# Performance work log

Hardware: AMD Instinct MI355X
Metric: run time of the kernel (lower is better)

Reference implementation:

```python
import jax, jax.numpy as jnp
import numpy as np

D_STATE = 128   # Mamba2 default (the SS2D d_state=16 is never forwarded to Mamba2)
N_HEADS = 4     # d_ssm // headdim = d_model / (d_model//4)
D_CONV = 4
EPS = 1e-5


def silu(v):
    return v * jax.nn.sigmoid(v)


def setup_inputs() -> dict:
    key = jax.random.key(0)
    ks = jax.random.split(key, 12)
    d_model = 256
    d_inner = 2 * d_model            # expand=2
    d_ssm = d_model
    conv_dim = d_ssm + 2 * D_STATE   # 512
    d_in_proj = 2 * d_inner + 2 * D_STATE + N_HEADS  # 1284
    B, H, W = 8, 64, 64
    inp = {
        "x": jax.random.normal(ks[0], (B, d_model, H, W), jnp.float32),
        "in_proj_w": jax.random.normal(ks[1], (d_in_proj, d_model), jnp.float32) * 0.02,
        "conv_w": jax.random.normal(ks[2], (conv_dim, D_CONV), jnp.float32) * 0.2,
        "conv_b": jnp.zeros((conv_dim,), jnp.float32),
        "dt_bias": jax.random.normal(ks[3], (N_HEADS,), jnp.float32) * 0.1,
        "A_log": jnp.log(jax.random.uniform(ks[4], (N_HEADS,), jnp.float32, 1.0, 16.0)),
        "D": jax.random.normal(ks[5], (N_HEADS,), jnp.float32),
        "norm_w": jnp.ones((d_ssm,), jnp.float32),
        "out_proj_w": jax.random.normal(ks[6], (d_model, d_inner), jnp.float32) * 0.02,
        "se_w1": jax.random.normal(ks[7], (d_model // 4, d_model), jnp.float32) * 0.05,
        "se_b1": jnp.zeros((d_model // 4,), jnp.float32),
        "se_w2": jax.random.normal(ks[8], (d_model, d_model // 4), jnp.float32) * 0.05,
        "se_b2": jnp.zeros((d_model,), jnp.float32),
    }
    return inp


def _forward(x, in_proj_w, conv_w, conv_b, dt_bias, A_log, D, norm_w,
             out_proj_w, se_w1, se_b1, se_w2, se_b2):
    Bb, C, H, W = x.shape
    L = H * W
    d_model = C
    d_inner = 2 * d_model
    d_ssm = d_model
    d_mlp = d_inner - d_ssm
    headdim = d_ssm // N_HEADS
    conv_dim = d_ssm + 2 * D_STATE

    u = x.reshape(Bb, C, L).transpose(0, 2, 1)              # (b, l, c)
    zxbcdt = u @ in_proj_w.T                                 # (b, l, 1284)
    z0 = zxbcdt[..., :d_mlp]
    x0 = zxbcdt[..., d_mlp:2 * d_mlp]
    z = zxbcdt[..., 2 * d_mlp:2 * d_mlp + d_ssm]
    xBC = zxbcdt[..., 2 * d_mlp + d_ssm:2 * d_mlp + d_ssm + conv_dim]
    dt = zxbcdt[..., -N_HEADS:]

    dt = jax.nn.softplus(dt + dt_bias)                       # (b, l, h)

    # causal depthwise conv along l, kernel size D_CONV
    xpad = jnp.pad(xBC, ((0, 0), (D_CONV - 1, 0), (0, 0)))
    xconv = conv_b
    for k in range(D_CONV):
        xconv = xconv + xpad[:, k:k + L, :] * conv_w[:, k]
    xconv = silu(xconv)

    xs = xconv[..., :d_ssm]
    Bm = xconv[..., d_ssm:d_ssm + D_STATE]                   # (b, l, n) ngroups=1
    Cm = xconv[..., d_ssm + D_STATE:]                        # (b, l, n)
    xh = xs.reshape(Bb, L, N_HEADS, headdim)                 # (b, l, h, p)

    A = -jnp.exp(A_log)                                      # (h,)

    def step(hstate, inp):
        xt, dtt, Bt, Ct = inp  # (b,h,p), (b,h), (b,n), (b,n)
        dA = jnp.exp(dtt * A)                                # (b, h)
        hstate = hstate * dA[:, :, None, None] + \
            (dtt[:, :, None, None] * xt[..., None]) * Bt[:, None, None, :]
        y = jnp.einsum('bhpn,bn->bhp', hstate, Ct)
        return hstate, y

    h0 = jnp.zeros((Bb, N_HEADS, headdim, D_STATE), x.dtype)
    _, ys = jax.lax.scan(
        step, h0,
        (xh.transpose(1, 0, 2, 3), dt.transpose(1, 0, 2),
         Bm.transpose(1, 0, 2), Cm.transpose(1, 0, 2)))
    y = ys.transpose(1, 0, 2, 3)                             # (b, l, h, p)
    y = y + D[None, None, :, None] * xh                      # skip
    y = y.reshape(Bb, L, d_ssm)

    # gated RMSNorm (norm_before_gate=False): gate then normalize
    y = y * silu(z)
    y = y * jax.lax.rsqrt(jnp.mean(y * y, axis=-1, keepdims=True) + EPS) * norm_w

    y = jnp.concatenate([silu(z0) * x0, y], axis=-1)         # (b, l, d_inner)
    out = y @ out_proj_w.T                                   # (b, l, d_model)
    out = out.transpose(0, 2, 1).reshape(Bb, C, H, W)

    # SE-style spectral attention
    s = out.mean(axis=(2, 3))                                # (b, c)
    s = jax.nn.relu(s @ se_w1.T + se_b1)
    s = jax.nn.sigmoid(s @ se_w2.T + se_b2)
    return out * s[:, :, None, None]


def reference(x, in_proj_w, conv_w, conv_b, dt_bias, A_log, D, norm_w,
              out_proj_w, se_w1, se_b1, se_w2, se_b2):
    return _forward(x, in_proj_w, conv_w, conv_b, dt_bias, A_log, D, norm_w,
                    out_proj_w, se_w1, se_b1, se_w2, se_b2)
```

## Files before the change

kernel.cpp:

```cpp
#include <hip/hip_runtime.h>
#include <stdint.h>

typedef __attribute__((ext_vector_type(8))) short bf16x8;
typedef __attribute__((ext_vector_type(4))) float f32x4;

__device__ __forceinline__ float bf2f(unsigned short u) {
  unsigned int x = ((unsigned int)u) << 16;
  return __builtin_bit_cast(float, x);
}
__device__ __forceinline__ unsigned short f2bf(float f) {
  unsigned int x = __builtin_bit_cast(unsigned int, f);
  unsigned int r = x + 0x7FFFu + ((x >> 16) & 1u);
  return (unsigned short)(r >> 16);
}
__device__ __forceinline__ float silu(float v) { return v / (1.f + expf(-v)); }
__device__ __forceinline__ f32x4 fz4() { f32x4 z; z[0]=0.f; z[1]=0.f; z[2]=0.f; z[3]=0.f; return z; }

#define LSEQ 4096
#define DMODEL 256
#define NIN 1284
#define NINP 1408

__global__ void k_prep_w(const float* __restrict__ w_in, const float* __restrict__ w_out,
                         unsigned short* __restrict__ wpad, unsigned short* __restrict__ woutbf) {
  int idx = blockIdx.x * 256 + threadIdx.x;
  const int tot1 = NINP * DMODEL;
  if (idx < tot1) {
    int n = idx / DMODEL, k = idx % DMODEL;
    float v = (n < NIN) ? w_in[n * DMODEL + k] : 0.f;
    wpad[idx] = f2bf(v);
  } else {
    int j = idx - tot1;
    woutbf[j] = f2bf(w_out[j]);
  }
}

__global__ __launch_bounds__(256) void k_transpose_x(const float* __restrict__ x,
                                                     unsigned short* __restrict__ ubf) {
  __shared__ float t[64][65];
  int bid = blockIdx.x;
  int b = bid >> 8;
  int r = bid & 255;
  int lt = r >> 2, kt = r & 3;
  int l0 = lt * 64, k0 = kt * 64;
  int tid = threadIdx.x;
  int j = tid & 63, i0 = tid >> 6;
  for (int rr = 0; rr < 16; rr++) {
    int ki = i0 + rr * 4;
    t[ki][j] = x[(size_t)(b * DMODEL + k0 + ki) * LSEQ + l0 + j];
  }
  __syncthreads();
  for (int rr = 0; rr < 16; rr++) {
    int li = i0 + rr * 4;
    ubf[(size_t)(b * LSEQ + l0 + li) * DMODEL + k0 + j] = f2bf(t[j][li]);
  }
}

template <int KDIM, int LDA, int LDB, int EPI>
__global__ __launch_bounds__(256) void k_gemm(const unsigned short* __restrict__ A,
                                              const unsigned short* __restrict__ B,
                                              float* __restrict__ outF,
                                              unsigned short* __restrict__ outBF,
                                              unsigned short* __restrict__ outBF2,
                                              float* __restrict__ dtb, int tilesN) {
  __shared__ __align__(16) short lds[17408];
  short* As = lds;
  short* Bs = lds + 8192;
  int nwg = gridDim.x;
  int orig = blockIdx.x;
  int wgid = (nwg & 7) ? orig : ((orig & 7) * (nwg >> 3) + (orig >> 3));
  int tn = wgid % tilesN, tm = wgid / tilesN;
  int m0 = tm * 128, n0 = tn * 128;
  int tid = threadIdx.x;
  int w = tid >> 6, lane = tid & 63;
  int wr = w >> 1, wc = w & 1;
  f32x4 acc[4][4];
  for (int i = 0; i < 4; i++)
    for (int j = 0; j < 4; j++) acc[i][j] = fz4();

  for (int kt = 0; kt < KDIM / 64; kt++) {
    int k0 = kt * 64;
    for (int i = 0; i < 4; i++) {
      int rowblk = w * 32 + i * 8;
      int row = rowblk + (lane >> 3);
      int kc = (lane & 7) * 8;
      const unsigned short* ga = A + (size_t)(m0 + row) * LDA + k0 + kc;
      __builtin_amdgcn_global_load_lds((const __attribute__((address_space(1))) unsigned int*)ga,
                                       (__attribute__((address_space(3))) unsigned int*)&As[rowblk * 64],
                                       16, 0, 0);
      const unsigned short* gb = B + (size_t)(n0 + row) * LDB + k0 + kc;
      __builtin_amdgcn_global_load_lds((const __attribute__((address_space(1))) unsigned int*)gb,
                                       (__attribute__((address_space(3))) unsigned int*)&Bs[rowblk * 64],
                                       16, 0, 0);
    }
    __syncthreads();
    for (int kk = 0; kk < 64; kk += 32) {
      bf16x8 af[4], bfr[4];
      for (int mi = 0; mi < 4; mi++)
        af[mi] = *(const bf16x8*)&As[(wr * 64 + mi * 16 + (lane & 15)) * 64 + kk + (lane >> 4) * 8];
      for (int ni = 0; ni < 4; ni++)
        bfr[ni] = *(const bf16x8*)&Bs[(wc * 64 + ni * 16 + (lane & 15)) * 64 + kk + (lane >> 4) * 8];
      for (int mi = 0; mi < 4; mi++)
        for (int ni = 0; ni < 4; ni++)
          acc[mi][ni] = __builtin_amdgcn_mfma_f32_16x16x32_bf16(af[mi], bfr[ni], acc[mi][ni], 0, 0, 0);
    }
    __syncthreads();
  }

  int fq = lane >> 4, fr = lane & 15;
  if constexpr (EPI == 1) {
    float* Cf = (float*)lds;
    for (int ph = 0; ph < 2; ph++) {
      if (ph) __syncthreads();
      if (wc == ph) {
        for (int mi = 0; mi < 4; mi++)
          for (int ni = 0; ni < 4; ni++)
            for (int j = 0; j < 4; j++)
              Cf[(wr * 64 + mi * 16 + fq * 4 + j) * 68 + ni * 16 + fr] = acc[mi][ni][j];
      }
      __syncthreads();
      int rr = tid >> 4, cc = (tid & 15) * 4;
      for (int it = 0; it < 8; it++) {
        int r = it * 16 + rr;
        float4 v = *(const float4*)&Cf[r * 68 + cc];
        *(float4*)&outF[(size_t)(m0 + r) * 256 + n0 + ph * 64 + cc] = v;
      }
    }
  } else {
    bool dttile = (n0 >= 1280);
    if (dttile) {
      if (wc == 0 && fr < 4) {
        for (int mi = 0; mi < 4; mi++)
          for (int j = 0; j < 4; j++) {
            int m = m0 + wr * 64 + mi * 16 + fq * 4 + j;
            dtb[m * 4 + fr] = acc[mi][0][j];
          }
      }
    } else {
      short* Ct = lds;
      for (int mi = 0; mi < 4; mi++)
        for (int ni = 0; ni < 4; ni++)
          for (int j = 0; j < 4; j++)
            Ct[(wr * 64 + mi * 16 + fq * 4 + j) * 136 + wc * 64 + ni * 16 + fr] =
                (short)f2bf(acc[mi][ni][j]);
      __syncthreads();
      int rr = tid >> 4, cc = (tid & 15) * 8;
      for (int it = 0; it < 8; it++) {
        int r = it * 16 + rr;
        uint4 v = *(const uint4*)&Ct[r * 136 + cc];
        if constexpr (EPI == 0) {
          *(uint4*)&outBF[(size_t)(m0 + r) * 1280 + n0 + cc] = v;
        } else {
          if (n0 < 768) *(uint4*)&outBF[(size_t)(m0 + r) * 768 + n0 + cc] = v;
          else *(uint4*)&outBF2[(size_t)(m0 + r) * 512 + (n0 - 768) + cc] = v;
        }
      }
    }
  }
}

__global__ __launch_bounds__(256) void k_conv(const unsigned short* __restrict__ src, int stride,
                                              const float* __restrict__ conv_w,
                                              const float* __restrict__ conv_b,
                                              unsigned short* __restrict__ xs,
                                              unsigned short* __restrict__ bc) {
  __shared__ __align__(16) unsigned short xt[35 * 512];
  int bid = blockIdx.x;
  int b = bid >> 7;
  int t0 = (bid & 127) * 32;
  int tid = threadIdx.x;
  for (int id = tid; id < 35 * 64; id += 256) {
    int r = id >> 6, ch = id & 63;
    int t = t0 - 3 + r;
    float4 v;
    if (t < 0) v = make_float4(0.f, 0.f, 0.f, 0.f);
    else v = *(const float4*)&src[(size_t)(b * LSEQ + t) * stride + ch * 8];
    *(float4*)&xt[r * 512 + ch * 8] = v;
  }
  __syncthreads();
  int c0 = tid, c1 = tid + 256;
  float w0[4], w1[4];
  for (int k = 0; k < 4; k++) { w0[k] = conv_w[c0 * 4 + k]; w1[k] = conv_w[c1 * 4 + k]; }
  float bb0 = conv_b[c0], bb1 = conv_b[c1];
  for (int tl = 0; tl < 32; tl++) {
    float a0 = bb0, a1 = bb1;
    for (int k = 0; k < 4; k++) {
      a0 += bf2f(xt[(tl + k) * 512 + c0]) * w0[k];
      a1 += bf2f(xt[(tl + k) * 512 + c1]) * w1[k];
    }
    a0 = silu(a0); a1 = silu(a1);
    size_t row = (size_t)(b * LSEQ + t0 + tl);
    xs[row * 256 + c0] = f2bf(a0);
    bc[row * 256 + (c1 - 256)] = f2bf(a1);
  }
}

__global__ __launch_bounds__(256) void k_scan(const unsigned short* __restrict__ xs,
                                              const unsigned short* __restrict__ bc,
                                              const float* __restrict__ dtb,
                                              const float* __restrict__ dt_bias,
                                              const float* __restrict__ A_log,
                                              const float* __restrict__ Dp,
                                              unsigned short* __restrict__ y) {
  __shared__ __align__(16) unsigned short bcl[32 * 256];
  __shared__ float xsl[32][4];
  __shared__ float dtl[32], dal[32];
  int bid = blockIdx.x;
  int b = bid >> 6;
  int h = (bid >> 4) & 3;
  int pg = bid & 15;
  int tid = threadIdx.x, w = tid >> 6, lane = tid & 63;
  int p = pg * 4 + w;
  float Ah = -expf(A_log[h]);
  float Dh = Dp[h];
  float bias = dt_bias[h];
  float h0 = 0.f, h1 = 0.f;
  for (int t0 = 0; t0 < LSEQ; t0 += 32) {
    for (int id = tid; id < 32 * 32; id += 256) {
      int r = id >> 5, ch = id & 31;
      *(float4*)&bcl[r * 256 + ch * 8] =
          *(const float4*)&bc[(size_t)(b * LSEQ + t0 + r) * 256 + ch * 8];
    }
    if (tid < 128) {
      int r = tid >> 2, pp = tid & 3;
      xsl[r][pp] = bf2f(xs[(size_t)(b * LSEQ + t0 + r) * 256 + h * 64 + pg * 4 + pp]);
    } else if (tid < 160) {
      int r = tid - 128;
      float v = dtb[(size_t)(b * LSEQ + t0 + r) * 4 + h] + bias;
      float dt = (v > 20.f) ? v : log1pf(expf(v));
      dtl[r] = dt;
      dal[r] = expf(dt * Ah);
    }
    __syncthreads();
    for (int tl = 0; tl < 32; tl++) {
      float dtv = dtl[tl], dav = dal[tl], xv = xsl[tl][w];
      float bn  = bf2f(bcl[tl * 256 + lane]);
      float bn2 = bf2f(bcl[tl * 256 + 64 + lane]);
      float cn  = bf2f(bcl[tl * 256 + 128 + lane]);
      float cn2 = bf2f(bcl[tl * 256 + 192 + lane]);
      float coef = dtv * xv;
      h0 = h0 * dav + coef * bn;
      h1 = h1 * dav + coef * bn2;
      float part = h0 * cn + h1 * cn2;
      for (int off = 32; off; off >>= 1) part += __shfl_xor(part, off, 64);
      if (lane == 0)
        y[(size_t)(b * LSEQ + t0 + tl) * 256 + h * 64 + p] = f2bf(part + Dh * xv);
    }
    __syncthreads();
  }
}

__global__ __launch_bounds__(64) void k_dtpre(const float* __restrict__ dtraw,
                                              const float* __restrict__ dt_bias,
                                              const float* __restrict__ A_log,
                                              float* __restrict__ dts, float* __restrict__ cums) {
  int bid = blockIdx.x;
  int bh = bid >> 6, c = bid & 63;
  int b = bh >> 2, h = bh & 3;
  int lane = threadIdx.x;
  int t = c * 64 + lane;
  float v = dtraw[(size_t)(b * LSEQ + t) * 4 + h] + dt_bias[h];
  float dt = (v > 20.f) ? v : log1pf(expf(v));
  float Ah = -expf(A_log[h]);
  float s = dt * Ah;
  for (int off = 1; off < 64; off <<= 1) {
    float o = __shfl_up(s, off, 64);
    if (lane >= off) s += o;
  }
  dts[bh * LSEQ + t] = dt;
  cums[bh * LSEQ + t] = s;
}

__global__ __launch_bounds__(256) void k_chunkA(const unsigned short* __restrict__ bc,
                                                const unsigned short* __restrict__ xs,
                                                const float* __restrict__ dts,
                                                const float* __restrict__ cums,
                                                float* __restrict__ ST,
                                                unsigned short* __restrict__ yb) {
  __shared__ __align__(16) unsigned short Cs[64 * 128];
  __shared__ __align__(16) unsigned short Bsm[64 * 128];
  __shared__ __align__(16) unsigned short Bt[128 * 64];
  __shared__ __align__(16) unsigned short Xt[64 * 64];
  __shared__ __align__(16) unsigned short Ms[64 * 72];
  __shared__ float dtl[64], cuml[64];
  int bid = blockIdx.x;
  int bh = bid >> 6, c = bid & 63;
  int b = bh >> 2, h = bh & 3;
  int m0 = b * LSEQ + c * 64;
  int tid = threadIdx.x, w = tid >> 6, lane = tid & 63;

  if (tid < 64) {
    dtl[tid] = dts[bh * LSEQ + c * 64 + tid];
    cuml[tid] = cums[bh * LSEQ + c * 64 + tid];
  }
  __syncthreads();
  float cumQ = cuml[63];

  for (int it = 0; it < 4; it++) {
    int idx = it * 256 + tid;
    int row = idx >> 4, g = idx & 15;
    int sg = g ^ (row & 7);
    uint4 vC = *(const uint4*)&bc[(size_t)(m0 + row) * 256 + 128 + g * 8];
    *(uint4*)((char*)Cs + row * 256 + sg * 16) = vC;
    uint4 vB = *(const uint4*)&bc[(size_t)(m0 + row) * 256 + g * 8];
    *(uint4*)((char*)Bsm + row * 256 + sg * 16) = vB;
    float sc = dtl[row] * expf(cumQ - cuml[row]);
    const unsigned short* pv = (const unsigned short*)&vB;
    for (int e = 0; e < 8; e++) {
      int n = g * 8 + e;
      *(unsigned short*)((char*)Bt + n * 128 + (((row >> 3) ^ (n & 7)) << 4) + ((row & 7) << 1)) =
          f2bf(bf2f(pv[e]) * sc);
    }
  }
  for (int it = 0; it < 2; it++) {
    int idx = it * 256 + tid;
    int row = idx >> 3, g = idx & 7;
    uint4 vX = *(const uint4*)&xs[(size_t)(m0 + row) * 256 + h * 64 + g * 8];
    const unsigned short* pv = (const unsigned short*)&vX;
    for (int e = 0; e < 8; e++) {
      int p = g * 8 + e;
      *(unsigned short*)((char*)Xt + p * 128 + (((row >> 3) ^ (p & 7)) << 4) + ((row & 7) << 1)) = pv[e];
    }
  }
  __syncthreads();

  f32x4 acc1[4];
#pragma unroll
  for (int i = 0; i < 4; i++) acc1[i] = fz4();
#pragma unroll
  for (int ks = 0; ks < 4; ks++) {
    int g = ks * 4 + (lane >> 4);
    int rt = w * 16 + (lane & 15);
    bf16x8 a = *(const bf16x8*)((char*)Cs + rt * 256 + ((g ^ (rt & 7)) << 4));
#pragma unroll
    for (int ni = 0; ni < 4; ni++) {
      int rs = ni * 16 + (lane & 15);
      bf16x8 bfr = *(const bf16x8*)((char*)Bsm + rs * 256 + ((g ^ (rs & 7)) << 4));
      acc1[ni] = __builtin_amdgcn_mfma_f32_16x16x32_bf16(a, bfr, acc1[ni], 0, 0, 0);
    }
  }
#pragma unroll
  for (int ni = 0; ni < 4; ni++)
#pragma unroll
    for (int j = 0; j < 4; j++) {
      int t = w * 16 + (lane >> 4) * 4 + j;
      int s = ni * 16 + (lane & 15);
      float v = 0.f;
      if (t >= s) v = acc1[ni][j] * expf(cuml[t] - cuml[s]) * dtl[s];
      *(unsigned short*)((char*)Ms + t * 128 + (((s >> 3) ^ (t & 7)) << 4) + ((s & 7) << 1)) = f2bf(v);
    }
  __syncthreads();

  f32x4 acc2[4], acc3[8];
#pragma unroll
  for (int i = 0; i < 4; i++) acc2[i] = fz4();
#pragma unroll
  for (int i = 0; i < 8; i++) acc3[i] = fz4();
#pragma unroll
  for (int ks = 0; ks < 2; ks++) {
    int g = ks * 4 + (lane >> 4);
    bf16x8 xf[4];
#pragma unroll
    for (int ni = 0; ni < 4; ni++) {
      int rp = ni * 16 + (lane & 15);
      xf[ni] = *(const bf16x8*)((char*)Xt + rp * 128 + ((g ^ (rp & 7)) << 4));
    }
    {
      int rt = w * 16 + (lane & 15);
      bf16x8 a = *(const bf16x8*)((char*)Ms + rt * 128 + ((g ^ (rt & 7)) << 4));
#pragma unroll
      for (int ni = 0; ni < 4; ni++)
        acc2[ni] = __builtin_amdgcn_mfma_f32_16x16x32_bf16(a, xf[ni], acc2[ni], 0, 0, 0);
    }
    {
      bf16x8 a3 = xf[w];
#pragma unroll
      for (int ni = 0; ni < 8; ni++) {
        int rn = ni * 16 + (lane & 15);
        bf16x8 bfr = *(const bf16x8*)((char*)Bt + rn * 128 + ((g ^ (rn & 7)) << 4));
        acc3[ni] = __builtin_amdgcn_mfma_f32_16x16x32_bf16(a3, bfr, acc3[ni], 0, 0, 0);
      }
    }
  }
  __syncthreads();
#pragma unroll
  for (int ni = 0; ni < 4; ni++)
#pragma unroll
    for (int j = 0; j < 4; j++) {
      int t = w * 16 + (lane >> 4) * 4 + j;
      int p = ni * 16 + (lane & 15);
      Ms[t * 72 + p] = f2bf(acc2[ni][j]);
    }
  float* stp = ST + ((size_t)bid << 13);
#pragma unroll
  for (int ni = 0; ni < 8; ni++)
#pragma unroll
    for (int j = 0; j < 4; j++) {
      int p = w * 16 + (lane >> 4) * 4 + j;
      int n = ni * 16 + (lane & 15);
      stp[p * 128 + n] = acc3[ni][j];
    }
  __syncthreads();
  {
    int rr = tid >> 3, cc = (tid & 7) * 8;
    for (int it = 0; it < 2; it++) {
      int t = it * 32 + rr;
      uint4 v = *(const uint4*)&Ms[t * 72 + cc];
      *(uint4*)&yb[(size_t)(m0 + t) * 256 + h * 64 + cc] = v;
    }
  }
}

__global__ __launch_bounds__(256) void k_chunkB(const float* __restrict__ ST,
                                                const float* __restrict__ cums,
                                                unsigned short* __restrict__ HT) {
  int bid = blockIdx.x;
  int bh = bid >> 3, psl = bid & 7;
  int p = psl * 8 + (threadIdx.x >> 5);
  int n0 = (threadIdx.x & 31) * 4;
  float H[4] = {0.f, 0.f, 0.f, 0.f};
  for (int c = 0; c < 64; c++) {
    size_t base = (size_t)(bh * 64 + c);
    ushort4 hv;
    unsigned short* ha = (unsigned short*)&hv;
#pragma unroll
    for (int e = 0; e < 4; e++) ha[e] = f2bf(H[e]);
    *(ushort4*)&HT[(base * 64 + p) * 128 + n0] = hv;
    float4 s4 = *(const float4*)&ST[(base << 13) + p * 128 + n0];
    float dec = expf(cums[bh * LSEQ + c * 64 + 63]);
    H[0] = H[0] * dec + s4.x;
    H[1] = H[1] * dec + s4.y;
    H[2] = H[2] * dec + s4.z;
    H[3] = H[3] * dec + s4.w;
  }
}

__global__ __launch_bounds__(256) void k_chunkC(const unsigned short* __restrict__ bc,
                                                const unsigned short* __restrict__ xs,
                                                const unsigned short* __restrict__ HT,
                                                const float* __restrict__ cums,
                                                const float* __restrict__ Dp,
                                                unsigned short* __restrict__ yb) {
  __shared__ __align__(16) unsigned short Cse[64 * 128];
  __shared__ __align__(16) unsigned short Hs[64 * 128];
  __shared__ __align__(16) unsigned short yst[64 * 72];
  int bid = blockIdx.x;
  int bh = bid >> 6, c = bid & 63;
  int b = bh >> 2, h = bh & 3;
  int m0 = b * LSEQ + c * 64;
  int tid = threadIdx.x, w = tid >> 6, lane = tid & 63;
  float Dh = Dp[h];
  for (int it = 0; it < 4; it++) {
    int idx = it * 256 + tid;
    int row = idx >> 4, g = idx & 15;
    int sg = g ^ (row & 7);
    float ex = expf(cums[bh * LSEQ + c * 64 + row]);
    uint4 vC = *(const uint4*)&bc[(size_t)(m0 + row) * 256 + 128 + g * 8];
    const unsigned short* pc = (const unsigned short*)&vC;
    uint4 vo;
    unsigned short* po = (unsigned short*)&vo;
#pragma unroll
    for (int e = 0; e < 8; e++) po[e] = f2bf(bf2f(pc[e]) * ex);
    *(uint4*)((char*)Cse + row * 256 + sg * 16) = vo;
    uint4 vH = *(const uint4*)&HT[((size_t)(bh * 64 + c) * 64 + row) * 128 + g * 8];
    *(uint4*)((char*)Hs + row * 256 + sg * 16) = vH;
  }
  __syncthreads();
  f32x4 acc[4];
#pragma unroll
  for (int i = 0; i < 4; i++) acc[i] = fz4();
#pragma unroll
  for (int ks = 0; ks < 4; ks++) {
    int g = ks * 4 + (lane >> 4);
    int rt = w * 16 + (lane & 15);
    bf16x8 a = *(const bf16x8*)((char*)Cse + rt * 256 + ((g ^ (rt & 7)) << 4));
#pragma unroll
    for (int ni = 0; ni < 4; ni++) {
      int rp = ni * 16 + (lane & 15);
      bf16x8 bfr = *(const bf16x8*)((char*)Hs + rp * 256 + ((g ^ (rp & 7)) << 4));
      acc[ni] = __builtin_amdgcn_mfma_f32_16x16x32_bf16(a, bfr, acc[ni], 0, 0, 0);
    }
  }
#pragma unroll
  for (int ni = 0; ni < 4; ni++)
#pragma unroll
    for (int j = 0; j < 4; j++) {
      int t = w * 16 + (lane >> 4) * 4 + j;
      int p = ni * 16 + (lane & 15);
      yst[t * 72 + p] = f2bf(acc[ni][j]);
    }
  __syncthreads();
  {
    int rr = tid >> 3, cc = (tid & 7) * 8;
    for (int it = 0; it < 2; it++) {
      int t = it * 32 + rr;
      size_t off = (size_t)(m0 + t) * 256 + h * 64 + cc;
      uint4 yo = *(const uint4*)&yb[off];
      uint4 xv = *(const uint4*)&xs[off];
      const unsigned short* pyo = (const unsigned short*)&yo;
      const unsigned short* pxv = (const unsigned short*)&xv;
      const unsigned short* pys = &yst[t * 72 + cc];
      uint4 vo;
      unsigned short* po = (unsigned short*)&vo;
#pragma unroll
      for (int e = 0; e < 8; e++)
        po[e] = f2bf(bf2f(pyo[e]) + bf2f(pys[e]) + Dh * bf2f(pxv[e]));
      *(uint4*)&yb[off] = vo;
    }
  }
}

__global__ __launch_bounds__(256) void k_ycat(const unsigned short* __restrict__ y,
                                              const unsigned short* __restrict__ zsrc, int zstride,
                                              const float* __restrict__ norm_w,
                                              unsigned short* __restrict__ ycat) {
  int bid = blockIdx.x;
  int tid = threadIdx.x, w = tid >> 6, lane = tid & 63;
  size_t m = (size_t)bid * 4 + w;
  int j0 = lane * 4;
  ushort4 yv = *(const ushort4*)&y[m * 256 + j0];
  ushort4 zv = *(const ushort4*)&zsrc[m * zstride + 512 + j0];
  unsigned short ya[4] = {yv.x, yv.y, yv.z, yv.w};
  unsigned short za[4] = {zv.x, zv.y, zv.z, zv.w};
  float g[4]; float ssum = 0.f;
  for (int i = 0; i < 4; i++) {
    float gg = bf2f(ya[i]) * silu(bf2f(za[i]));
    g[i] = gg; ssum += gg * gg;
  }
  for (int off = 32; off; off >>= 1) ssum += __shfl_xor(ssum, off, 64);
  float inv = rsqrtf(ssum * (1.f / 256.f) + 1e-5f);
  ushort4 z0v = *(const ushort4*)&zsrc[m * zstride + j0];
  ushort4 x0v = *(const ushort4*)&zsrc[m * zstride + 256 + j0];
  unsigned short z0a[4] = {z0v.x, z0v.y, z0v.z, z0v.w};
  unsigned short x0a[4] = {x0v.x, x0v.y, x0v.z, x0v.w};
  ushort4 o1, o2;
  unsigned short* o1a = (unsigned short*)&o1;
  unsigned short* o2a = (unsigned short*)&o2;
  for (int i = 0; i < 4; i++) {
    o1a[i] = f2bf(silu(bf2f(z0a[i])) * bf2f(x0a[i]));
    o2a[i] = f2bf(g[i] * norm_w[j0 + i] * inv);
  }
  *(ushort4*)&ycat[m * 512 + j0] = o1;
  *(ushort4*)&ycat[m * 512 + 256 + j0] = o2;
}

__global__ void k_zero(float* __restrict__ p) { p[blockIdx.x * 256 + threadIdx.x] = 0.f; }

__global__ __launch_bounds__(256) void k_semean(const float* __restrict__ res, float* __restrict__ smean) {
  int bid = blockIdx.x;
  int b = bid >> 5, ch = bid & 31;
  int c = threadIdx.x;
  float acc = 0.f;
  for (int r = 0; r < 128; r++)
    acc += res[(size_t)(b * LSEQ + ch * 128 + r) * 256 + c];
  atomicAdd(&smean[b * 256 + c], acc);
}

__global__ __launch_bounds__(512) void k_sefc(const float* __restrict__ smean,
                                              const float* __restrict__ w1, const float* __restrict__ b1,
                                              const float* __restrict__ w2, const float* __restrict__ b2,
                                              float* __restrict__ s2) {
  __shared__ float s1[512];
  int tid = threadIdx.x;
  int b = tid >> 6, j = tid & 63;
  float acc = b1[j];
  for (int k = 0; k < 256; k++) acc += smean[b * 256 + k] * (1.f / 4096.f) * w1[j * 256 + k];
  s1[b * 64 + j] = fmaxf(acc, 0.f);
  __syncthreads();
  for (int idx = tid; idx < 2048; idx += 512) {
    int bb = idx >> 8, c = idx & 255;
    float a2 = b2[c];
    for (int k = 0; k < 64; k++) a2 += s1[bb * 64 + k] * w2[c * 64 + k];
    s2[idx] = 1.f / (1.f + expf(-a2));
  }
}

__global__ __launch_bounds__(256) void k_final(const float* __restrict__ res,
                                               const float* __restrict__ s2,
                                               float* __restrict__ out) {
  __shared__ float t[64][65];
  int bid = blockIdx.x;
  int b = bid >> 8;
  int r = bid & 255;
  int ct = r >> 6, lt = r & 63;
  int c0 = ct * 64, l0 = lt * 64;
  int tid = threadIdx.x, j = tid & 63, i0 = tid >> 6;
  for (int rr = 0; rr < 16; rr++) {
    int i = i0 + rr * 4;
    t[i][j] = res[(size_t)(b * LSEQ + l0 + i) * 256 + c0 + j];
  }
  __syncthreads();
  for (int rr = 0; rr < 16; rr++) {
    int ci = i0 + rr * 4;
    float s = s2[b * 256 + c0 + ci];
    out[(size_t)(b * 256 + c0 + ci) * LSEQ + l0 + j] = t[j][ci] * s;
  }
}

extern "C" void kernel_launch(void* const* d_in, const int* in_sizes, int n_in,
                              void* d_out, int out_size, void* d_ws, size_t ws_size,
                              hipStream_t stream) {
  const float* x         = (const float*)d_in[0];
  const float* in_proj_w = (const float*)d_in[1];
  const float* conv_w    = (const float*)d_in[2];
  const float* conv_b    = (const float*)d_in[3];
  const float* dt_bias   = (const float*)d_in[4];
  const float* A_log     = (const float*)d_in[5];
  const float* Dp        = (const float*)d_in[6];
  const float* norm_w    = (const float*)d_in[7];
  const float* out_projw = (const float*)d_in[8];
  const float* se_w1     = (const float*)d_in[9];
  const float* se_b1     = (const float*)d_in[10];
  const float* se_w2     = (const float*)d_in[11];
  const float* se_b2     = (const float*)d_in[12];
  float* out = (float*)d_out;
  char* ws = (char*)d_ws;

  const size_t NEED_CHUNKED = 220676096;

  if (ws_size >= NEED_CHUNKED) {
    unsigned short* ubf   = (unsigned short*)(ws + 0);
    unsigned short* xbc   = (unsigned short*)(ws + 16777216);
    unsigned short* ycat  = (unsigned short*)(ws + 50331648);
    float*          ST    = (float*)(ws + 0);
    float*          res   = (float*)(ws + 0);
    unsigned short* zxa   = (unsigned short*)(ws + 83886080);
    unsigned short* xsb   = (unsigned short*)(ws + 134217728);
    unsigned short* bcb   = (unsigned short*)(ws + 150994944);
    unsigned short* HT    = (unsigned short*)(ws + 167772160);
    unsigned short* ybuf  = (unsigned short*)(ws + 201326592);
    unsigned short* wpad  = (unsigned short*)(ws + 218103808);
    unsigned short* woutb = (unsigned short*)(ws + 218824704);
    float*          dtraw = (float*)(ws + 219086848);
    float*          dts   = (float*)(ws + 219611136);
    float*          cums  = (float*)(ws + 220135424);
    float*          smean = (float*)(ws + 220659712);
    float*          s2    = (float*)(ws + 220667904);

    k_prep_w<<<1920, 256, 0, stream>>>(in_proj_w, out_projw, wpad, woutb);
    k_transpose_x<<<2048, 256, 0, stream>>>(x, ubf);
    k_gemm<256, 256, 256, 2><<<256 * 11, 256, 0, stream>>>(ubf, wpad, nullptr, zxa, xbc, dtraw, 11);
    k_conv<<<1024, 256, 0, stream>>>(xbc, 512, conv_w, conv_b, xsb, bcb);
    k_dtpre<<<2048, 64, 0, stream>>>(dtraw, dt_bias, A_log, dts, cums);
    k_chunkA<<<2048, 256, 0, stream>>>(bcb, xsb, dts, cums, ST, ybuf);
    k_chunkB<<<256, 256, 0, stream>>>(ST, cums, HT);
    k_chunkC<<<2048, 256, 0, stream>>>(bcb, xsb, HT, cums, Dp, ybuf);
    k_ycat<<<8192, 256, 0, stream>>>(ybuf, zxa, 768, norm_w, ycat);
    k_gemm<512, 512, 512, 1><<<256 * 2, 256, 0, stream>>>(ycat, woutb, res, nullptr, nullptr, nullptr, 2);
    k_zero<<<8, 256, 0, stream>>>(smean);
    k_semean<<<256, 256, 0, stream>>>(res, smean);
    k_sefc<<<1, 512, 0, stream>>>(smean, se_w1, se_b1, se_w2, se_b2, s2);
    k_final<<<2048, 256, 0, stream>>>(res, s2, out);
  } else {
    unsigned short* ubf   = (unsigned short*)(ws + 0);
    unsigned short* xsb   = (unsigned short*)(ws + 16777216);
    float*          res   = (float*)(ws + 0);
    unsigned short* bcb   = (unsigned short*)(ws + 33554432);
    unsigned short* zx    = (unsigned short*)(ws + 50331648);
    float*          dtb   = (float*)(ws + 134217728);
    unsigned short* ybuf  = (unsigned short*)(ws + 134742016);
    unsigned short* ycat  = (unsigned short*)(ws + 151519232);
    unsigned short* wpad  = (unsigned short*)(ws + 185073664);
    unsigned short* woutb = (unsigned short*)(ws + 185794560);
    float*          smean = (float*)(ws + 186056704);
    float*          s2    = (float*)(ws + 186064896);

    k_prep_w<<<1920, 256, 0, stream>>>(in_proj_w, out_projw, wpad, woutb);
    k_transpose_x<<<2048, 256, 0, stream>>>(x, ubf);
    k_gemm<256, 256, 256, 0><<<256 * 11, 256, 0, stream>>>(ubf, wpad, nullptr, zx, nullptr, dtb, 11);
    k_conv<<<1024, 256, 0, stream>>>(zx + 768, 1280, conv_w, conv_b, xsb, bcb);
    k_scan<<<512, 256, 0, stream>>>(xsb, bcb, dtb, dt_bias, A_log, Dp, ybuf);
    k_ycat<<<8192, 256, 0, stream>>>(ybuf, zx, 1280, norm_w, ycat);
    k_gemm<512, 512, 512, 1><<<256 * 2, 256, 0, stream>>>(ycat, woutb, res, nullptr, nullptr, nullptr, 2);
    k_zero<<<8, 256, 0, stream>>>(smean);
    k_semean<<<256, 256, 0, stream>>>(res, smean);
    k_sefc<<<1, 512, 0, stream>>>(smean, se_w1, se_b1, se_w2, se_b2, s2);
    k_final<<<2048, 256, 0, stream>>>(res, s2, out);
  }
}
```

Measured before the change: 252.2 us.

## Fuse SiLU gating into in_proj epilogue and pre-transpose conv outputs for chunk scan

```diff
diff --git a/kernel.cpp b/kernel.cpp
--- a/kernel.cpp
+++ b/kernel.cpp
@@ -13,7 +13,7 @@
   unsigned int r = x + 0x7FFFu + ((x >> 16) & 1u);
   return (unsigned short)(r >> 16);
 }
-__device__ __forceinline__ float silu(float v) { return v / (1.f + expf(-v)); }
+__device__ __forceinline__ float silu(float v) { return v / (1.f + __expf(-v)); }
 __device__ __forceinline__ f32x4 fz4() { f32x4 z; z[0]=0.f; z[1]=0.f; z[2]=0.f; z[3]=0.f; return z; }
 
 #define LSEQ 4096
@@ -27,7 +27,8 @@
   const int tot1 = NINP * DMODEL;
   if (idx < tot1) {
     int n = idx / DMODEL, k = idx % DMODEL;
-    float v = (n < NIN) ? w_in[n * DMODEL + k] : 0.f;
+    int src = (n < 512) ? ((n & 1) ? 256 + (n >> 1) : (n >> 1)) : n;
+    float v = (src < NIN) ? w_in[src * DMODEL + k] : 0.f;
     wpad[idx] = f2bf(v);
   } else {
     int j = idx - tot1;
@@ -124,6 +125,52 @@
         int r = it * 16 + rr;
         float4 v = *(const float4*)&Cf[r * 68 + cc];
         *(float4*)&outF[(size_t)(m0 + r) * 256 + n0 + ph * 64 + cc] = v;
+      }
+    }
+  } else if constexpr (EPI == 2) {
+    unsigned short* xbc = (unsigned short*)outF;
+    if (n0 >= 1280) {
+      if (wc == 0 && fr < 4) {
+        for (int mi = 0; mi < 4; mi++)
+          for (int j = 0; j < 4; j++) {
+            int m = m0 + wr * 64 + mi * 16 + fq * 4 + j;
+            dtb[m * 4 + fr] = acc[mi][0][j];
+          }
+      }
+    } else if (n0 < 512) {
+      short* Ct = lds;
+      for (int mi = 0; mi < 4; mi++)
+        for (int ni = 0; ni < 4; ni++)
+          for (int j = 0; j < 4; j++) {
+            float v = acc[mi][ni][j];
+            float vp = __shfl_xor(v, 1, 64);
+            if (!(fr & 1)) {
+              float zc = silu(v) * vp;
+              Ct[(wr * 64 + mi * 16 + fq * 4 + j) * 72 + wc * 32 + ni * 8 + (fr >> 1)] =
+                  (short)f2bf(zc);
+            }
+          }
+      __syncthreads();
+      int r = tid >> 1, base = (tid & 1) * 32;
+      for (int it = 0; it < 4; it++) {
+        int cc = base + it * 8;
+        uint4 v = *(const uint4*)&Ct[r * 72 + cc];
+        *(uint4*)&outBF[(size_t)(m0 + r) * 512 + (n0 >> 1) + cc] = v;
+      }
+    } else {
+      short* Ct = lds;
+      for (int mi = 0; mi < 4; mi++)
+        for (int ni = 0; ni < 4; ni++)
+          for (int j = 0; j < 4; j++)
+            Ct[(wr * 64 + mi * 16 + fq * 4 + j) * 136 + wc * 64 + ni * 16 + fr] =
+                (short)f2bf(acc[mi][ni][j]);
+      __syncthreads();
+      int rr = tid >> 4, cc = (tid & 15) * 8;
+      for (int it = 0; it < 8; it++) {
+        int r = it * 16 + rr;
+        uint4 v = *(const uint4*)&Ct[r * 136 + cc];
+        if (n0 < 768) *(uint4*)&outBF2[(size_t)(m0 + r) * 256 + (n0 - 512) + cc] = v;
+        else *(uint4*)&xbc[(size_t)(m0 + r) * 512 + (n0 - 768) + cc] = v;
       }
     }
   } else {
@@ -148,12 +195,7 @@
       for (int it = 0; it < 8; it++) {
         int r = it * 16 + rr;
         uint4 v = *(const uint4*)&Ct[r * 136 + cc];
-        if constexpr (EPI == 0) {
-          *(uint4*)&outBF[(size_t)(m0 + r) * 1280 + n0 + cc] = v;
-        } else {
-          if (n0 < 768) *(uint4*)&outBF[(size_t)(m0 + r) * 768 + n0 + cc] = v;
-          else *(uint4*)&outBF2[(size_t)(m0 + r) * 512 + (n0 - 768) + cc] = v;
-        }
+        *(uint4*)&outBF[(size_t)(m0 + r) * 1280 + n0 + cc] = v;
       }
     }
   }
@@ -163,7 +205,9 @@
                                               const float* __restrict__ conv_w,
                                               const float* __restrict__ conv_b,
                                               unsigned short* __restrict__ xs,
-                                              unsigned short* __restrict__ bc) {
+                                              unsigned short* __restrict__ bc,
+                                              unsigned short* __restrict__ xsT,
+                                              unsigned short* __restrict__ bT) {
   __shared__ __align__(16) unsigned short xt[35 * 512];
   int bid = blockIdx.x;
   int b = bid >> 7;
@@ -182,6 +226,8 @@
   float w0[4], w1[4];
   for (int k = 0; k < 4; k++) { w0[k] = conv_w[c0 * 4 + k]; w1[k] = conv_w[c1 * 4 + k]; }
   float bb0 = conv_b[c0], bb1 = conv_b[c1];
+  unsigned short xa0[32], xa1[32];
+#pragma unroll
   for (int tl = 0; tl < 32; tl++) {
     float a0 = bb0, a1 = bb1;
     for (int k = 0; k < 4; k++) {
@@ -189,9 +235,21 @@
       a1 += bf2f(xt[(tl + k) * 512 + c1]) * w1[k];
     }
     a0 = silu(a0); a1 = silu(a1);
+    unsigned short u0 = f2bf(a0), u1 = f2bf(a1);
+    xa0[tl] = u0; xa1[tl] = u1;
     size_t row = (size_t)(b * LSEQ + t0 + tl);
-    xs[row * 256 + c0] = f2bf(a0);
-    bc[row * 256 + (c1 - 256)] = f2bf(a1);
+    xs[row * 256 + c0] = u0;
+    bc[row * 256 + (c1 - 256)] = u1;
+  }
+  if (xsT) {
+    const uint4* p0 = (const uint4*)xa0;
+    for (int k = 0; k < 4; k++)
+      *(uint4*)&xsT[((size_t)(b * 256 + c0)) * LSEQ + t0 + k * 8] = p0[k];
+    if (c1 < 384) {
+      const uint4* p1 = (const uint4*)xa1;
+      for (int k = 0; k < 4; k++)
+        *(uint4*)&bT[((size_t)(b * 128 + (c1 - 256))) * LSEQ + t0 + k * 8] = p1[k];
+    }
   }
 }
 
@@ -272,17 +330,17 @@
 }
 
 __global__ __launch_bounds__(256) void k_chunkA(const unsigned short* __restrict__ bc,
-                                                const unsigned short* __restrict__ xs,
+                                                const unsigned short* __restrict__ xsT,
+                                                const unsigned short* __restrict__ bT,
                                                 const float* __restrict__ dts,
                                                 const float* __restrict__ cums,
                                                 float* __restrict__ ST,
                                                 unsigned short* __restrict__ yb) {
-  __shared__ __align__(16) unsigned short Cs[64 * 128];
   __shared__ __align__(16) unsigned short Bsm[64 * 128];
-  __shared__ __align__(16) unsigned short Bt[128 * 64];
-  __shared__ __align__(16) unsigned short Xt[64 * 64];
+  __shared__ __align__(16) unsigned short BTs[128 * 64];
+  __shared__ __align__(16) unsigned short XT[64 * 64];
   __shared__ __align__(16) unsigned short Ms[64 * 72];
-  __shared__ float dtl[64], cuml[64];
+  __shared__ float dtl[64], cuml[64], scl[64];
   int bid = blockIdx.x;
   int bh = bid >> 6, c = bid & 63;
   int b = bh >> 2, h = bh & 3;
@@ -297,41 +355,36 @@
   float cumQ = cuml[63];
 
   for (int it = 0; it < 4; it++) {
-    int idx = it * 256 + tid;
-    int row = idx >> 4, g = idx & 15;
-    int sg = g ^ (row & 7);
-    uint4 vC = *(const uint4*)&bc[(size_t)(m0 + row) * 256 + 128 + g * 8];
-    *(uint4*)((char*)Cs + row * 256 + sg * 16) = vC;
-    uint4 vB = *(const uint4*)&bc[(size_t)(m0 + row) * 256 + g * 8];
-    *(uint4*)((char*)Bsm + row * 256 + sg * 16) = vB;
-    float sc = dtl[row] * expf(cumQ - cuml[row]);
-    const unsigned short* pv = (const unsigned short*)&vB;
-    for (int e = 0; e < 8; e++) {
-      int n = g * 8 + e;
-      *(unsigned short*)((char*)Bt + n * 128 + (((row >> 3) ^ (n & 7)) << 4) + ((row & 7) << 1)) =
-          f2bf(bf2f(pv[e]) * sc);
-    }
+    int idx = it * 256 + tid, row = idx >> 4, g = idx & 15;
+    uint4 v = *(const uint4*)&bc[(size_t)(m0 + row) * 256 + g * 8];
+    *(uint4*)((char*)Bsm + row * 256 + ((g ^ (row & 7)) << 4)) = v;
   }
   for (int it = 0; it < 2; it++) {
-    int idx = it * 256 + tid;
-    int row = idx >> 3, g = idx & 7;
-    uint4 vX = *(const uint4*)&xs[(size_t)(m0 + row) * 256 + h * 64 + g * 8];
-    const unsigned short* pv = (const unsigned short*)&vX;
-    for (int e = 0; e < 8; e++) {
-      int p = g * 8 + e;
-      *(unsigned short*)((char*)Xt + p * 128 + (((row >> 3) ^ (p & 7)) << 4) + ((row & 7) << 1)) = pv[e];
-    }
-  }
-  __syncthreads();
-
+    int idx = it * 256 + tid, row = idx >> 3, g = idx & 7;
+    uint4 v = *(const uint4*)&xsT[((size_t)(b * 256 + h * 64 + row)) * LSEQ + c * 64 + g * 8];
+    *(uint4*)((char*)XT + row * 128 + ((g ^ (row & 7)) << 4)) = v;
+  }
+  if (tid < 64) scl[tid] = dtl[tid] * __expf(cumQ - cuml[tid]);
+  __syncthreads();
+  for (int it = 0; it < 4; it++) {
+    int idx = it * 256 + tid, row = idx >> 3, g = idx & 7;
+    uint4 v = *(const uint4*)&bT[((size_t)(b * 128 + row)) * LSEQ + c * 64 + g * 8];
+    const unsigned short* pv = (const unsigned short*)&v;
+    uint4 o; unsigned short* po = (unsigned short*)&o;
+#pragma unroll
+    for (int e = 0; e < 8; e++) po[e] = f2bf(bf2f(pv[e]) * scl[g * 8 + e]);
+    *(uint4*)((char*)BTs + row * 128 + ((g ^ (row & 7)) << 4)) = o;
+  }
+
+  int rt = w * 16 + (lane & 15);
+  const unsigned short* arow = bc + (size_t)(m0 + rt) * 256 + 128;
   f32x4 acc1[4];
 #pragma unroll
   for (int i = 0; i < 4; i++) acc1[i] = fz4();
 #pragma unroll
   for (int ks = 0; ks < 4; ks++) {
     int g = ks * 4 + (lane >> 4);
-    int rt = w * 16 + (lane & 15);
-    bf16x8 a = *(const bf16x8*)((char*)Cs + rt * 256 + ((g ^ (rt & 7)) << 4));
+    bf16x8 a = *(const bf16x8*)&arow[g * 8];
 #pragma unroll
     for (int ni = 0; ni < 4; ni++) {
       int rs = ni * 16 + (lane & 15);
@@ -346,7 +399,7 @@
       int t = w * 16 + (lane >> 4) * 4 + j;
       int s = ni * 16 + (lane & 15);
       float v = 0.f;
-      if (t >= s) v = acc1[ni][j] * expf(cuml[t] - cuml[s]) * dtl[s];
+      if (t >= s) v = acc1[ni][j] * __expf(cuml[t] - cuml[s]) * dtl[s];
       *(unsigned short*)((char*)Ms + t * 128 + (((s >> 3) ^ (t & 7)) << 4) + ((s & 7) << 1)) = f2bf(v);
     }
   __syncthreads();
@@ -363,10 +416,9 @@
 #pragma unroll
     for (int ni = 0; ni < 4; ni++) {
       int rp = ni * 16 + (lane & 15);
-      xf[ni] = *(const bf16x8*)((char*)Xt + rp * 128 + ((g ^ (rp & 7)) << 4));
+      xf[ni] = *(const bf16x8*)((char*)XT + rp * 128 + ((g ^ (rp & 7)) << 4));
     }
     {
-      int rt = w * 16 + (lane & 15);
       bf16x8 a = *(const bf16x8*)((char*)Ms + rt * 128 + ((g ^ (rt & 7)) << 4));
 #pragma unroll
       for (int ni = 0; ni < 4; ni++)
@@ -377,7 +429,7 @@
 #pragma unroll
       for (int ni = 0; ni < 8; ni++) {
         int rn = ni * 16 + (lane & 15);
-        bf16x8 bfr = *(const bf16x8*)((char*)Bt + rn * 128 + ((g ^ (rn & 7)) << 4));
+        bf16x8 bfr = *(const bf16x8*)((char*)BTs + rn * 128 + ((g ^ (rn & 7)) << 4));
         acc3[ni] = __builtin_amdgcn_mfma_f32_16x16x32_bf16(a3, bfr, acc3[ni], 0, 0, 0);
       }
     }
@@ -427,7 +479,7 @@
     for (int e = 0; e < 4; e++) ha[e] = f2bf(H[e]);
     *(ushort4*)&HT[(base * 64 + p) * 128 + n0] = hv;
     float4 s4 = *(const float4*)&ST[(base << 13) + p * 128 + n0];
-    float dec = expf(cums[bh * LSEQ + c * 64 + 63]);
+    float dec = __expf(cums[bh * LSEQ + c * 64 + 63]);
     H[0] = H[0] * dec + s4.x;
     H[1] = H[1] * dec + s4.y;
     H[2] = H[2] * dec + s4.z;
@@ -441,7 +493,6 @@
                                                 const float* __restrict__ cums,
                                                 const float* __restrict__ Dp,
                                                 unsigned short* __restrict__ yb) {
-  __shared__ __align__(16) unsigned short Cse[64 * 128];
   __shared__ __align__(16) unsigned short Hs[64 * 128];
   __shared__ __align__(16) unsigned short yst[64 * 72];
   int bid = blockIdx.x;
@@ -451,29 +502,26 @@
   int tid = threadIdx.x, w = tid >> 6, lane = tid & 63;
   float Dh = Dp[h];
   for (int it = 0; it < 4; it++) {
-    int idx = it * 256 + tid;
-    int row = idx >> 4, g = idx & 15;
-    int sg = g ^ (row & 7);
-    float ex = expf(cums[bh * LSEQ + c * 64 + row]);
-    uint4 vC = *(const uint4*)&bc[(size_t)(m0 + row) * 256 + 128 + g * 8];
-    const unsigned short* pc = (const unsigned short*)&vC;
-    uint4 vo;
-    unsigned short* po = (unsigned short*)&vo;
-#pragma unroll
-    for (int e = 0; e < 8; e++) po[e] = f2bf(bf2f(pc[e]) * ex);
-    *(uint4*)((char*)Cse + row * 256 + sg * 16) = vo;
-    uint4 vH = *(const uint4*)&HT[((size_t)(bh * 64 + c) * 64 + row) * 128 + g * 8];
-    *(uint4*)((char*)Hs + row * 256 + sg * 16) = vH;
-  }
-  __syncthreads();
+    int idx = it * 256 + tid, row = idx >> 4, g = idx & 15;
+    uint4 v = *(const uint4*)&HT[((size_t)(bh * 64 + c) * 64 + row) * 128 + g * 8];
+    *(uint4*)((char*)Hs + row * 256 + ((g ^ (row & 7)) << 4)) = v;
+  }
+  float exq[4];
+  {
+    int tb = w * 16 + (lane >> 4) * 4;
+#pragma unroll
+    for (int j = 0; j < 4; j++) exq[j] = __expf(cums[bh * LSEQ + c * 64 + tb + j]);
+  }
+  __syncthreads();
+  int rt = w * 16 + (lane & 15);
+  const unsigned short* arow = bc + (size_t)(m0 + rt) * 256 + 128;
   f32x4 acc[4];
 #pragma unroll
   for (int i = 0; i < 4; i++) acc[i] = fz4();
 #pragma unroll
   for (int ks = 0; ks < 4; ks++) {
     int g = ks * 4 + (lane >> 4);
-    int rt = w * 16 + (lane & 15);
-    bf16x8 a = *(const bf16x8*)((char*)Cse + rt * 256 + ((g ^ (rt & 7)) << 4));
+    bf16x8 a = *(const bf16x8*)&arow[g * 8];
 #pragma unroll
     for (int ni = 0; ni < 4; ni++) {
       int rp = ni * 16 + (lane & 15);
@@ -487,7 +535,7 @@
     for (int j = 0; j < 4; j++) {
       int t = w * 16 + (lane >> 4) * 4 + j;
       int p = ni * 16 + (lane & 15);
-      yst[t * 72 + p] = f2bf(acc[ni][j]);
+      yst[t * 72 + p] = f2bf(acc[ni][j] * exq[j]);
     }
   __syncthreads();
   {
@@ -510,16 +558,19 @@
   }
 }
 
+template <int MODE>
 __global__ __launch_bounds__(256) void k_ycat(const unsigned short* __restrict__ y,
-                                              const unsigned short* __restrict__ zsrc, int zstride,
+                                              const unsigned short* __restrict__ zsrc,
                                               const float* __restrict__ norm_w,
-                                              unsigned short* __restrict__ ycat) {
+                                              unsigned short* __restrict__ ocat) {
   int bid = blockIdx.x;
   int tid = threadIdx.x, w = tid >> 6, lane = tid & 63;
   size_t m = (size_t)bid * 4 + w;
   int j0 = lane * 4;
   ushort4 yv = *(const ushort4*)&y[m * 256 + j0];
-  ushort4 zv = *(const ushort4*)&zsrc[m * zstride + 512 + j0];
+  ushort4 zv;
+  if constexpr (MODE == 0) zv = *(const ushort4*)&zsrc[m * 256 + j0];
+  else zv = *(const ushort4*)&zsrc[m * 1280 + 512 + j0];
   unsigned short ya[4] = {yv.x, yv.y, yv.z, yv.w};
   unsigned short za[4] = {zv.x, zv.y, zv.z, zv.w};
   float g[4]; float ssum = 0.f;
@@ -529,19 +580,21 @@
   }
   for (int off = 32; off; off >>= 1) ssum += __shfl_xor(ssum, off, 64);
   float inv = rsqrtf(ssum * (1.f / 256.f) + 1e-5f);
-  ushort4 z0v = *(const ushort4*)&zsrc[m * zstride + j0];
-  ushort4 x0v = *(const ushort4*)&zsrc[m * zstride + 256 + j0];
-  unsigned short z0a[4] = {z0v.x, z0v.y, z0v.z, z0v.w};
-  unsigned short x0a[4] = {x0v.x, x0v.y, x0v.z, x0v.w};
-  ushort4 o1, o2;
-  unsigned short* o1a = (unsigned short*)&o1;
+  ushort4 o2;
   unsigned short* o2a = (unsigned short*)&o2;
-  for (int i = 0; i < 4; i++) {
-    o1a[i] = f2bf(silu(bf2f(z0a[i])) * bf2f(x0a[i]));
-    o2a[i] = f2bf(g[i] * norm_w[j0 + i] * inv);
-  }
-  *(ushort4*)&ycat[m * 512 + j0] = o1;
-  *(ushort4*)&ycat[m * 512 + 256 + j0] = o2;
+  for (int i = 0; i < 4; i++) o2a[i] = f2bf(g[i] * norm_w[j0 + i] * inv);
+  *(ushort4*)&ocat[m * 512 + 256 + j0] = o2;
+  if constexpr (MODE == 1) {
+    ushort4 p0 = *(const ushort4*)&zsrc[m * 1280 + 2 * j0];
+    ushort4 p1 = *(const ushort4*)&zsrc[m * 1280 + 2 * j0 + 4];
+    ushort4 o1;
+    unsigned short* o1a = (unsigned short*)&o1;
+    o1a[0] = f2bf(silu(bf2f(p0.x)) * bf2f(p0.y));
+    o1a[1] = f2bf(silu(bf2f(p0.z)) * bf2f(p0.w));
+    o1a[2] = f2bf(silu(bf2f(p1.x)) * bf2f(p1.y));
+    o1a[3] = f2bf(silu(bf2f(p1.z)) * bf2f(p1.w));
+    *(ushort4*)&ocat[m * 512 + j0] = o1;
+  }
 }
 
 __global__ void k_zero(float* __restrict__ p) { p[blockIdx.x * 256 + threadIdx.x] = 0.f; }
@@ -619,34 +672,36 @@
   const size_t NEED_CHUNKED = 220676096;
 
   if (ws_size >= NEED_CHUNKED) {
+    float*          ST    = (float*)(ws + 0);
     unsigned short* ubf   = (unsigned short*)(ws + 0);
     unsigned short* xbc   = (unsigned short*)(ws + 16777216);
-    unsigned short* ycat  = (unsigned short*)(ws + 50331648);
-    float*          ST    = (float*)(ws + 0);
     float*          res   = (float*)(ws + 0);
-    unsigned short* zxa   = (unsigned short*)(ws + 83886080);
-    unsigned short* xsb   = (unsigned short*)(ws + 134217728);
-    unsigned short* bcb   = (unsigned short*)(ws + 150994944);
-    unsigned short* HT    = (unsigned short*)(ws + 167772160);
-    unsigned short* ybuf  = (unsigned short*)(ws + 201326592);
-    unsigned short* wpad  = (unsigned short*)(ws + 218103808);
-    unsigned short* woutb = (unsigned short*)(ws + 218824704);
-    float*          dtraw = (float*)(ws + 219086848);
-    float*          dts   = (float*)(ws + 219611136);
-    float*          cums  = (float*)(ws + 220135424);
-    float*          smean = (float*)(ws + 220659712);
-    float*          s2    = (float*)(ws + 220667904);
+    unsigned short* zcat  = (unsigned short*)(ws + 67108864);
+    unsigned short* zbuf  = (unsigned short*)(ws + 100663296);
+    unsigned short* xsb   = (unsigned short*)(ws + 117440512);
+    unsigned short* bcb   = (unsigned short*)(ws + 134217728);
+    unsigned short* HT    = (unsigned short*)(ws + 150994944);
+    unsigned short* xsT   = (unsigned short*)(ws + 150994944);
+    unsigned short* bT    = (unsigned short*)(ws + 167772160);
+    unsigned short* ybuf  = (unsigned short*)(ws + 184549376);
+    unsigned short* wpad  = (unsigned short*)(ws + 201326592);
+    unsigned short* woutb = (unsigned short*)(ws + 202047488);
+    float*          dtraw = (float*)(ws + 202309632);
+    float*          dts   = (float*)(ws + 202833920);
+    float*          cums  = (float*)(ws + 203358208);
+    float*          smean = (float*)(ws + 203882496);
+    float*          s2    = (float*)(ws + 203890688);
 
     k_prep_w<<<1920, 256, 0, stream>>>(in_proj_w, out_projw, wpad, woutb);
     k_transpose_x<<<2048, 256, 0, stream>>>(x, ubf);
-    k_gemm<256, 256, 256, 2><<<256 * 11, 256, 0, stream>>>(ubf, wpad, nullptr, zxa, xbc, dtraw, 11);
-    k_conv<<<1024, 256, 0, stream>>>(xbc, 512, conv_w, conv_b, xsb, bcb);
+    k_gemm<256, 256, 256, 2><<<256 * 11, 256, 0, stream>>>(ubf, wpad, (float*)xbc, zcat, zbuf, dtraw, 11);
+    k_conv<<<1024, 256, 0, stream>>>(xbc, 512, conv_w, conv_b, xsb, bcb, xsT, bT);
     k_dtpre<<<2048, 64, 0, stream>>>(dtraw, dt_bias, A_log, dts, cums);
-    k_chunkA<<<2048, 256, 0, stream>>>(bcb, xsb, dts, cums, ST, ybuf);
+    k_chunkA<<<2048, 256, 0, stream>>>(bcb, xsT, bT, dts, cums, ST, ybuf);
     k_chunkB<<<256, 256, 0, stream>>>(ST, cums, HT);
     k_chunkC<<<2048, 256, 0, stream>>>(bcb, xsb, HT, cums, Dp, ybuf);
-    k_ycat<<<8192, 256, 0, stream>>>(ybuf, zxa, 768, norm_w, ycat);
-    k_gemm<512, 512, 512, 1><<<256 * 2, 256, 0, stream>>>(ycat, woutb, res, nullptr, nullptr, nullptr, 2);
+    k_ycat<0><<<8192, 256, 0, stream>>>(ybuf, zbuf, norm_w, zcat);
+    k_gemm<512, 512, 512, 1><<<256 * 2, 256, 0, stream>>>(zcat, woutb, res, nullptr, nullptr, nullptr, 2);
     k_zero<<<8, 256, 0, stream>>>(smean);
     k_semean<<<256, 256, 0, stream>>>(res, smean);
     k_sefc<<<1, 512, 0, stream>>>(smean, se_w1, se_b1, se_w2, se_b2, s2);
@@ -668,9 +723,9 @@
     k_prep_w<<<1920, 256, 0, stream>>>(in_proj_w, out_projw, wpad, woutb);
     k_transpose_x<<<2048, 256, 0, stream>>>(x, ubf);
     k_gemm<256, 256, 256, 0><<<256 * 11, 256, 0, stream>>>(ubf, wpad, nullptr, zx, nullptr, dtb, 11);
-    k_conv<<<1024, 256, 0, stream>>>(zx + 768, 1280, conv_w, conv_b, xsb, bcb);
+    k_conv<<<1024, 256, 0, stream>>>(zx + 768, 1280, conv_w, conv_b, xsb, bcb, nullptr, nullptr);
     k_scan<<<512, 256, 0, stream>>>(xsb, bcb, dtb, dt_bias, A_log, Dp, ybuf);
-    k_ycat<<<8192, 256, 0, stream>>>(ybuf, zx, 1280, norm_w, ycat);
+    k_ycat<1><<<8192, 256, 0, stream>>>(ybuf, zx, norm_w, ycat);
     k_gemm<512, 512, 512, 1><<<256 * 2, 256, 0, stream>>>(ycat, woutb, res, nullptr, nullptr, nullptr, 2);
     k_zero<<<8, 256, 0, stream>>>(smean);
     k_semean<<<256, 256, 0, stream>>>(res, smean);
```

New measurement: 236.1 us. -6.4%, faster.
